# Performance work log

Hardware: AMD Instinct MI355X
Metric: run time of the kernel (lower is better)

Reference implementation:

```python
import jax, jax.numpy as jnp
import numpy as np

N_ENT = 500000   # entity vocab
N_REL = 500      # relation vocab
D = 128          # embed_size
H = 256          # hidden_size
B = 4096         # number of support pairs
NBR = 32         # neighbors per node
NODES = 2 * B
T = NODES * NBR  # total neighbor edges


def setup_inputs() -> dict:
    key = jax.random.key(0)
    ks = jax.random.split(key, 12)
    entities = jax.random.randint(ks[0], (NODES,), 0, N_ENT)
    neighbor_entities = jax.random.randint(ks[1], (T,), 0, N_ENT)
    neighbor_relations = jax.random.randint(ks[2], (T,), 0, N_REL)
    offsets = (jnp.arange(NODES) * NBR).astype(jnp.int64 if jax.config.read('jax_enable_x64') else jnp.int32)
    def init(k, shape, fan_in):
        return jax.random.normal(k, shape, dtype=jnp.float32) * (1.0 / np.sqrt(fan_in))
    return dict(
        entity_embeddings=init(ks[3], (N_ENT, D), D),
        relation_embeddings=init(ks[4], (N_REL, D), D),
        Wt=init(ks[5], (D, H), D),      bt=jnp.zeros((H,), jnp.float32),
        Wn=init(ks[6], (2 * D, H), 2 * D), bn=jnp.zeros((H,), jnp.float32),
        Wr=init(ks[7], (2 * H, H), 2 * H), br=jnp.zeros((H,), jnp.float32),
        entities=entities,
        neighbor_entities=neighbor_entities,
        neighbor_relations=neighbor_relations,
        offsets=offsets,
    )


def _segment_mean(table, idx, offsets, num_segments):
    # embedding_bag(mode='mean') with ragged offsets
    n = idx.shape[0]
    seg = jnp.searchsorted(offsets, jnp.arange(n), side='right') - 1   # [T] bag id per edge
    counts = jnp.diff(jnp.concatenate([offsets, jnp.array([n], offsets.dtype)]))
    summed = jax.ops.segment_sum(table[idx], seg, num_segments=num_segments)
    return summed / jnp.maximum(counts, 1).astype(table.dtype)[:, None]


def reference(entity_embeddings, relation_embeddings, Wt, bt, Wn, bn, Wr, br,
              entities, neighbor_entities, neighbor_relations, offsets):
    nodes = entities.shape[0]
    # self-entity transform
    ent = entity_embeddings[entities] @ Wt + bt                        # [2B, H]
    # neighbor mean-aggregation (entity + relation bags share offsets)
    ne = _segment_mean(entity_embeddings, neighbor_entities, offsets, nodes)    # [2B, D]
    nr = _segment_mean(relation_embeddings, neighbor_relations, offsets, nodes)  # [2B, D]
    nbr = jnp.concatenate([ne, nr], axis=-1) @ Wn + bn                 # [2B, H]
    node = jax.nn.relu(ent + nbr).reshape(nodes // 2, 2 * Wt.shape[1])  # [B, 2H]
    pair = jax.nn.relu(node @ Wr + br)                                 # [B, H]
    return pair
```

## Files before the change

### kernel.cpp

```cpp
#include <hip/hip_runtime.h>
#include <hip/hip_bf16.h>

#define N_ENT   500000
#define N_REL   500
#define D       128
#define H       256
#define NPAIR   4096
#define NBR     32
#define NODES   8192
#define T_EDGES 262144
#define K1      384
#define K2      512

typedef __bf16  bf16x8  __attribute__((ext_vector_type(8)));
typedef float   floatx4 __attribute__((ext_vector_type(4)));

__device__ inline unsigned short f2bf(float f) {
  unsigned u = __float_as_uint(f);
  unsigned r = (u + 0x7fffu + ((u >> 16) & 1u)) >> 16;
  return (unsigned short)r;
}

__global__ __launch_bounds__(128) void gather_kernel(
    const float* __restrict__ ent_emb, const float* __restrict__ rel_emb,
    const int* __restrict__ entities, const int* __restrict__ nbr_ent,
    const int* __restrict__ nbr_rel, const int* __restrict__ offsets,
    unsigned short* __restrict__ X)
{
  int n = blockIdx.x;
  int j = threadIdx.x;
  int self = entities[n];
  int beg = offsets[n];
  int end = (n + 1 < NODES) ? offsets[n + 1] : T_EDGES;
  int cnt = end - beg; if (cnt < 1) cnt = 1;

  float s = ent_emb[(long)self * D + j];
  float se = 0.f, sr = 0.f;
  for (int k = beg; k < end; ++k) {
    int ie = nbr_ent[k];
    int ir = nbr_rel[k];
    se += ent_emb[(long)ie * D + j];
    sr += rel_emb[(long)ir * D + j];
  }
  float inv = 1.f / (float)cnt;
  unsigned short* row = X + (long)n * K1;
  row[j]         = f2bf(s);
  row[D + j]     = f2bf(se * inv);
  row[2 * D + j] = f2bf(sr * inv);
}

__global__ __launch_bounds__(256) void prep_weights(
    const float* __restrict__ Wt, const float* __restrict__ Wn,
    const float* __restrict__ Wr,
    unsigned short* __restrict__ W1t, unsigned short* __restrict__ W2t)
{
  int idx = blockIdx.x * 256 + threadIdx.x;
  if (idx < H * K1) {
    int nn = idx / K1, k = idx % K1;
    float v = (k < D) ? Wt[k * H + nn] : Wn[(k - D) * H + nn];
    W1t[idx] = f2bf(v);
  }
  if (idx < H * K2) {
    int nn = idx / K2, k = idx % K2;
    W2t[idx] = f2bf(Wr[k * H + nn]);
  }
}

template<int K>
__global__ __launch_bounds__(256) void gemm_bias_relu(
    const bf16x8* __restrict__ A8,
    const bf16x8* __restrict__ Bt8,
    const float* __restrict__ bias0, const float* __restrict__ bias1,
    unsigned short* __restrict__ out_bf, float* __restrict__ out_f, int N)
{
  constexpr int K8 = K / 8;
  __shared__ bf16x8 Ash[64 * 4];
  __shared__ bf16x8 Bsh[64 * 4];

  int tid  = threadIdx.x;
  int wave = tid >> 6, lane = tid & 63;
  int quad = lane >> 4, l15 = lane & 15;
  int bm = blockIdx.x * 64, bn = blockIdx.y * 64;
  int r  = tid >> 2;
  int s4 = tid & 3;

  floatx4 acc[4];
  #pragma unroll
  for (int i = 0; i < 4; ++i) acc[i] = (floatx4){0.f, 0.f, 0.f, 0.f};

  for (int k0 = 0; k0 < K8; k0 += 4) {
    Ash[tid] = A8[(long)(bm + r) * K8 + k0 + s4];
    Bsh[tid] = Bt8[(long)(bn + r) * K8 + k0 + s4];
    __syncthreads();
    bf16x8 a = Ash[(wave * 16 + l15) * 4 + quad];
    #pragma unroll
    for (int nt = 0; nt < 4; ++nt) {
      bf16x8 b = Bsh[(nt * 16 + l15) * 4 + quad];
      acc[nt] = __builtin_amdgcn_mfma_f32_16x16x32_bf16(a, b, acc[nt], 0, 0, 0);
    }
    __syncthreads();
  }

  #pragma unroll
  for (int nt = 0; nt < 4; ++nt) {
    int gn = bn + nt * 16 + l15;
    float bs = bias0[gn] + (bias1 ? bias1[gn] : 0.f);
    #pragma unroll
    for (int i = 0; i < 4; ++i) {
      long gm = bm + wave * 16 + quad * 4 + i;
      float v = acc[nt][i] + bs;
      v = v > 0.f ? v : 0.f;
      if (out_bf) out_bf[gm * N + gn] = f2bf(v);
      else        out_f [gm * N + gn] = v;
    }
  }
}

extern "C" void kernel_launch(void* const* d_in, const int* in_sizes, int n_in,
                              void* d_out, int out_size, void* d_ws, size_t ws_size,
                              hipStream_t stream) {
  const float* ent_emb = (const float*)d_in[0];
  const float* rel_emb = (const float*)d_in[1];
  const float* Wt      = (const float*)d_in[2];
  const float* bt      = (const float*)d_in[3];
  const float* Wn      = (const float*)d_in[4];
  const float* bn      = (const float*)d_in[5];
  const float* Wr      = (const float*)d_in[6];
  const float* br      = (const float*)d_in[7];
  const int* entities  = (const int*)d_in[8];
  const int* nbr_ent   = (const int*)d_in[9];
  const int* nbr_rel   = (const int*)d_in[10];
  const int* offsets   = (const int*)d_in[11];

  char* ws = (char*)d_ws;
  unsigned short* X    = (unsigned short*)(ws);
  unsigned short* node = (unsigned short*)(ws + 6291456);
  unsigned short* W1t  = (unsigned short*)(ws + 10485760);
  unsigned short* W2t  = (unsigned short*)(ws + 10682368);

  gather_kernel<<<dim3(NODES), dim3(128), 0, stream>>>(
      ent_emb, rel_emb, entities, nbr_ent, nbr_rel, offsets, X);

  prep_weights<<<dim3((H * K2 + 255) / 256), dim3(256), 0, stream>>>(
      Wt, Wn, Wr, W1t, W2t);

  gemm_bias_relu<K1><<<dim3(NODES / 64, H / 64), dim3(256), 0, stream>>>(
      (const bf16x8*)X, (const bf16x8*)W1t, bt, bn,
      node, (float*)nullptr, H);

  gemm_bias_relu<K2><<<dim3(NPAIR / 64, H / 64), dim3(256), 0, stream>>>(
      (const bf16x8*)node, (const bf16x8*)W2t, br, (const float*)nullptr,
      (unsigned short*)nullptr, (float*)d_out, H);
}
```

Measured before the change: 374.6 us.

## Restructure gather to one wave per node with float2 loads and batched prefetch

The gather kernel now assigns one 64-lane wave per node, four nodes per block, and each lane loads float2 instead of one float. When a node has exactly NBR neighbours, all neighbour indices are loaded up front and the embedding rows are fetched in batches of eight, so many independent loads are in flight at once. This targets the latency-bound serial loop of dependent index-then-row loads. Holding the unrolled index and row arrays raises register use, and nodes with other neighbour counts fall back to the serial loop.

After: 358.3 us. 4.4% less time.

```diff
diff --git a/kernel.cpp b/kernel.cpp
--- a/kernel.cpp
+++ b/kernel.cpp
@@ -21,32 +21,66 @@
   return (unsigned short)r;
 }
 
-__global__ __launch_bounds__(128) void gather_kernel(
+__global__ __launch_bounds__(256) void gather_kernel(
     const float* __restrict__ ent_emb, const float* __restrict__ rel_emb,
     const int* __restrict__ entities, const int* __restrict__ nbr_ent,
     const int* __restrict__ nbr_rel, const int* __restrict__ offsets,
     unsigned short* __restrict__ X)
 {
-  int n = blockIdx.x;
-  int j = threadIdx.x;
-  int self = entities[n];
+  int wave = threadIdx.x >> 6;
+  int lane = threadIdx.x & 63;
+  int n = blockIdx.x * 4 + wave;
+
   int beg = offsets[n];
   int end = (n + 1 < NODES) ? offsets[n + 1] : T_EDGES;
-  int cnt = end - beg; if (cnt < 1) cnt = 1;
+  int cnt = end - beg;
 
-  float s = ent_emb[(long)self * D + j];
-  float se = 0.f, sr = 0.f;
-  for (int k = beg; k < end; ++k) {
-    int ie = nbr_ent[k];
-    int ir = nbr_rel[k];
-    se += ent_emb[(long)ie * D + j];
-    sr += rel_emb[(long)ir * D + j];
+  const float2* ent2 = (const float2*)ent_emb;
+  const float2* rel2 = (const float2*)rel_emb;
+
+  int self = entities[n];
+  float2 s = ent2[(long)self * 64 + lane];
+
+  float sex = 0.f, sey = 0.f, srx = 0.f, sry = 0.f;
+
+  if (cnt == NBR) {
+    int ie[NBR], ir[NBR];
+    #pragma unroll
+    for (int k = 0; k < NBR; ++k) ie[k] = nbr_ent[beg + k];
+    #pragma unroll
+    for (int k = 0; k < NBR; ++k) ir[k] = nbr_rel[beg + k];
+
+    #pragma unroll
+    for (int c = 0; c < NBR / 8; ++c) {
+      float2 e[8], r[8];
+      #pragma unroll
+      for (int j = 0; j < 8; ++j) e[j] = ent2[(long)ie[c * 8 + j] * 64 + lane];
+      #pragma unroll
+      for (int j = 0; j < 8; ++j) r[j] = rel2[(long)ir[c * 8 + j] * 64 + lane];
+      #pragma unroll
+      for (int j = 0; j < 8; ++j) {
+        sex += e[j].x; sey += e[j].y;
+        srx += r[j].x; sry += r[j].y;
+      }
+    }
+  } else {
+    for (int k = beg; k < end; ++k) {
+      float2 e = ent2[(long)nbr_ent[k] * 64 + lane];
+      float2 r = rel2[(long)nbr_rel[k] * 64 + lane];
+      sex += e.x; sey += e.y; srx += r.x; sry += r.y;
+    }
   }
-  float inv = 1.f / (float)cnt;
+
+  int cc = cnt < 1 ? 1 : cnt;
+  float inv = 1.f / (float)cc;
+
   unsigned short* row = X + (long)n * K1;
-  row[j]         = f2bf(s);
-  row[D + j]     = f2bf(se * inv);
-  row[2 * D + j] = f2bf(sr * inv);
+  ushort2* p0 = (ushort2*)(row) + lane;
+  ushort2* p1 = (ushort2*)(row + D) + lane;
+  ushort2* p2 = (ushort2*)(row + 2 * D) + lane;
+  *p0 = make_ushort2(f2bf(s.x), f2bf(s.y));
+  *p1 = make_ushort2(f2bf(sex * inv), f2bf(sey * inv));
+  *p2 = make_ushort2(f2bf(srx * inv), f2bf(sry * inv));
 }
 
 __global__ __launch_bounds__(256) void prep_weights(
@@ -138,7 +172,7 @@
   unsigned short* W1t  = (unsigned short*)(ws + 10485760);
   unsigned short* W2t  = (unsigned short*)(ws + 10682368);
 
-  gather_kernel<<<dim3(NODES), dim3(128), 0, stream>>>(
+  gather_kernel<<<dim3(NODES / 4), dim3(256), 0, stream>>>(
       ent_emb, rel_emb, entities, nbr_ent, nbr_rel, offsets, X);
 
   prep_weights<<<dim3((H * K2 + 255) / 256), dim3(256), 0, stream>>>(
```
